# Kernel tuning notes

Hardware: AMD Instinct MI355X
Metric: run time of the kernel (lower is better)

Reference implementation:

```python
import jax, jax.numpy as jnp
import numpy as np
from jax import lax

N, P = 64, 7
C1, H1 = 256, 56
C2, H2 = 512, 28
C3, H3 = 1024, 14
HID1, HID2, HID3 = 256, 768, 1792
MLP1, MLP2, OUT = 3584, 1792, 512


def setup_inputs() -> dict:
    key = jax.random.key(0)
    ks = jax.random.split(key, 32)
    x1 = jax.random.normal(ks[0], (N, C1, H1, H1), jnp.float32)
    x2 = jax.random.normal(ks[1], (N, C2, H2, H2), jnp.float32)
    x3 = jax.random.normal(ks[2], (N, C3, H3, H3), jnp.float32)
    a = jax.random.randint(ks[3], (N, P, 2), 0, 56)
    b = jax.random.randint(ks[4], (N, P, 2), 0, 56)
    lo, hi = jnp.minimum(a, b), jnp.maximum(a, b)
    patchs = jnp.stack([lo[..., 0], hi[..., 0], lo[..., 1], hi[..., 1]], axis=-1)
    drop = jax.random.bernoulli(ks[5], 0.1, (N, P))
    patchs = jnp.where(drop[..., None], 0, patchs).astype(jnp.int32)

    def lin(k, o, i):
        return jax.random.normal(k, (o, i), jnp.float32) * 0.02

    def vec(k, o):
        return jax.random.normal(k, (o,), jnp.float32) * 0.02

    inp = {
        'x1': x1, 'x2': x2, 'x3': x3, 'patchs': patchs,
        # LSTM weights, torch gate order (i,f,g,o); bias = b_ih + b_hh combined
        'l1_wih': lin(ks[6], 4 * HID1, 256),  'l1_whh': lin(ks[7], 4 * HID1, HID1),  'l1_b': vec(ks[8], 4 * HID1),
        'l2_wih': lin(ks[9], 4 * HID2, 768),  'l2_whh': lin(ks[10], 4 * HID2, HID2), 'l2_b': vec(ks[11], 4 * HID2),
        'l3_wih': lin(ks[12], 4 * HID3, 1792),'l3_whh': lin(ks[13], 4 * HID3, HID3), 'l3_b': vec(ks[14], 4 * HID3),
        'aw1': lin(ks[15], MLP1, P * HID3), 'ab1': vec(ks[16], MLP1),
        'aw2': lin(ks[17], MLP2, MLP1),     'ab2': vec(ks[18], MLP2),
        'aw3': lin(ks[19], P, MLP2),        'ab3': vec(ks[20], P),
        'fw':  lin(ks[21], OUT, HID3),      'fb':  vec(ks[22], OUT),
    }
    return inp


def _crop_avg(x, patchs, num, den):
    """Batched data-dependent crop + avg-pool via 2D integral image.
    x: [N,C,H,W]; patchs: [N,P,4] ints (y0,y1,x0,x1) at 56-scale. Returns [N,P,C]."""
    y0 = (patchs[..., 0] * num) // den
    y1 = (patchs[..., 1] * num) // den
    x0 = (patchs[..., 2] * num) // den
    x1 = (patchs[..., 3] * num) // den
    S = jnp.cumsum(jnp.cumsum(x, axis=2), axis=3)
    S = jnp.pad(S, ((0, 0), (0, 0), (1, 0), (1, 0)))  # [N,C,H+1,W+1]
    bidx = jnp.arange(x.shape[0])[:, None]

    def g(Y, X):
        return S[bidx, :, Y, X]  # advanced idx split by ':' -> [N,P,C]

    tot = g(y1 + 1, x1 + 1) - g(y0, x1 + 1) - g(y1 + 1, x0) + g(y0, x0)
    area = ((y1 - y0 + 1) * (x1 - x0 + 1)).astype(x.dtype)[..., None]
    avg = tot / area
    zero = jnp.all(patchs == 0, axis=-1)  # all-zero box -> zero feature
    return jnp.where(zero[..., None], jnp.zeros((), x.dtype), avg)


def _lstm(x, wih, whh, b):
    """Single-layer batch-first LSTM, torch gate order i,f,g,o. x: [N,T,D] -> [N,T,H]."""
    Nb, T, _ = x.shape
    H = whh.shape[1]
    xg = jnp.einsum('ntd,gd->ntg', x, wih) + b  # precompute input gates

    def step(carry, xt):
        h, c = carry
        gates = xt + h @ whh.T
        i, f, g, o = jnp.split(gates, 4, axis=-1)
        c = jax.nn.sigmoid(f) * c + jax.nn.sigmoid(i) * jnp.tanh(g)
        h = jax.nn.sigmoid(o) * jnp.tanh(c)
        return (h, c), h

    h0 = jnp.zeros((Nb, H), x.dtype)
    _, hs = lax.scan(step, (h0, h0), jnp.swapaxes(xg, 0, 1))
    return jnp.swapaxes(hs, 0, 1)


def reference(x1, x2, x3, patchs,
              l1_wih, l1_whh, l1_b, l2_wih, l2_whh, l2_b, l3_wih, l3_whh, l3_b,
              aw1, ab1, aw2, ab2, aw3, ab3, fw, fb):
    local1 = _crop_avg(x1, patchs, 55, 55)                     # [N,7,256]
    rnn1 = _lstm(local1, l1_wih, l1_whh, l1_b)                 # [N,7,256]
    local2 = jnp.concatenate([_crop_avg(x2, patchs, 27, 55), rnn1], axis=2)   # [N,7,768]
    rnn2 = _lstm(local2, l2_wih, l2_whh, l2_b)                 # [N,7,768]
    local3 = jnp.concatenate([_crop_avg(x3, patchs, 13, 55), rnn2], axis=2)   # [N,7,1792]
    rnn3 = _lstm(local3, l3_wih, l3_whh, l3_b)                 # [N,7,1792]
    # attention pooling (dropout = identity in eval)
    flat = rnn3.reshape(rnn3.shape[0], -1)                     # [N,7*1792]
    h = jax.nn.relu(flat @ aw1.T + ab1)
    h = jax.nn.relu(h @ aw2.T + ab2)
    attn = jax.nn.relu(h @ aw3.T + ab3)                        # [N,7]
    alpha = jax.nn.softmax(attn, axis=1)
    feat = jnp.sum(rnn3 * alpha[:, :, None], axis=1)           # [N,1792]
    return feat @ fw.T + fb                                    # [N,512]
```

## Files before the change

kernel.cpp:

```cpp
#include <hip/hip_runtime.h>
#include <hip/hip_bf16.h>
#include <math.h>

#define NB 64
#define PP 7

typedef __attribute__((ext_vector_type(8))) short short8;
typedef __attribute__((ext_vector_type(4))) float f32x4;

static __device__ inline unsigned bf16r(float f) {
    unsigned u = __builtin_bit_cast(unsigned, f);
    u += 0x7fffu + ((u >> 16) & 1u);
    return u >> 16;
}
static __device__ inline unsigned pack2(float a, float b) {
    return bf16r(a) | (bf16r(b) << 16);
}

template<int H, int VEC, int GRP>
__device__ inline void crop_dev(
    int bx, int n, const float* __restrict__ x, const int* __restrict__ patchs,
    float* __restrict__ out, int C, int num, int den, int ldo, int col0)
{
    constexpr int USED = H / VEC;
    constexpr int PPWAVE = 64 / GRP;
    int tid = threadIdx.x, lane = tid & 63, wv = tid >> 6;
    int sub = lane / GRP, xl = lane & (GRP - 1);
    bool act = xl < USED;
    int c = bx * (4 * PPWAVE) + wv * PPWAVE + sub;

    int y0m1[PP], y1s[PP], x0s[PP], x1s[PP], zer[PP];
    float rarea[PP];
    #pragma unroll
    for (int p = 0; p < PP; ++p) {
        int p0 = patchs[(n * PP + p) * 4 + 0];
        int p1 = patchs[(n * PP + p) * 4 + 1];
        int p2 = patchs[(n * PP + p) * 4 + 2];
        int p3 = patchs[(n * PP + p) * 4 + 3];
        int y0 = p0 * num / den, y1 = p1 * num / den;
        int xx0 = p2 * num / den, xx1 = p3 * num / den;
        y0m1[p] = y0 - 1; y1s[p] = y1; x0s[p] = xx0; x1s[p] = xx1;
        rarea[p] = 1.f / (float)((y1 - y0 + 1) * (xx1 - xx0 + 1));
        zer[p] = (p0 | p1 | p2 | p3) == 0;
    }

    const float* pl = x + ((size_t)n * C + c) * (H * H) + (act ? xl * VEC : 0);

    float cc[VEC];
    float lo[PP][VEC], hi[PP][VEC];
    #pragma unroll
    for (int e = 0; e < VEC; ++e) cc[e] = 0.f;
    #pragma unroll
    for (int p = 0; p < PP; ++p)
        #pragma unroll
        for (int e = 0; e < VEC; ++e) { lo[p][e] = 0.f; hi[p][e] = 0.f; }

    #pragma unroll 4
    for (int y = 0; y < H; ++y) {
        float v[VEC];
        if constexpr (VEC == 4) {
            float4 t = *reinterpret_cast<const float4*>(pl + y * H);
            v[0] = t.x; v[1] = t.y; v[2] = t.z; v[3] = t.w;
        } else {
            float2 t = *reinterpret_cast<const float2*>(pl + y * H);
            v[0] = t.x; v[1] = t.y;
        }
        #pragma unroll
        for (int e = 0; e < VEC; ++e) cc[e] += v[e];
        #pragma unroll
        for (int p = 0; p < PP; ++p) {
            #pragma unroll
            for (int e = 0; e < VEC; ++e) {
                lo[p][e] = (y == y0m1[p]) ? cc[e] : lo[p][e];
                hi[p][e] = (y == y1s[p]) ? cc[e] : hi[p][e];
            }
        }
    }

    #pragma unroll
    for (int p = 0; p < PP; ++p) {
        float d = 0.f;
        #pragma unroll
        for (int e = 0; e < VEC; ++e) {
            int col = xl * VEC + e;
            if (col >= x0s[p] && col <= x1s[p]) d += hi[p][e] - lo[p][e];
        }
        #pragma unroll
        for (int off = GRP / 2; off >= 1; off >>= 1)
            d += __shfl_xor(d, off, 64);
        if (act && xl == 0)
            out[(size_t)(n * PP + p) * ldo + col0 + c] = zer[p] ? 0.f : d * rarea[p];
    }
}

__device__ inline void cvt_dev(
    int b, const float* __restrict__ in, uint4* __restrict__ out, int n8)
{
    int idx = b * 256 + threadIdx.x;
    if (idx >= n8) return;
    const float4* p = reinterpret_cast<const float4*>(in) + 2 * (size_t)idx;
    float4 a = p[0], bb = p[1];
    uint4 v;
    v.x = pack2(a.x, a.y); v.y = pack2(a.z, a.w);
    v.z = pack2(bb.x, bb.y); v.w = pack2(bb.z, bb.w);
    out[idx] = v;
}

__global__ __launch_bounds__(256) void prep_kernel(
    const float* __restrict__ x1, const float* __restrict__ x2,
    const float* __restrict__ x3, const int* __restrict__ patchs,
    float* __restrict__ local1, float* __restrict__ local2,
    float* __restrict__ local3,
    const float* __restrict__ l1_whh, uint4* __restrict__ whh1b,
    const float* __restrict__ l2_whh, uint4* __restrict__ whh2b,
    const float* __restrict__ l3_whh, uint4* __restrict__ whh3b)
{
    int b = blockIdx.x;
    if (b < 1024) {
        crop_dev<56, 4, 16>(b & 15, b >> 4, x1, patchs, local1, 256, 55, 55, 256, 0);
    } else if (b < 2048) {
        int bb = b - 1024;
        crop_dev<28, 4, 8>(bb & 15, bb >> 4, x2, patchs, local2, 512, 27, 55, 768, 0);
    } else if (b < 4096) {
        int bb = b - 2048;
        crop_dev<14, 2, 8>(bb & 31, bb >> 5, x3, patchs, local3, 1024, 13, 55, 1792, 0);
    } else if (b < 4224) {
        cvt_dev(b - 4096, l1_whh, whh1b, 32768);
    } else if (b < 5376) {
        cvt_dev(b - 4224, l2_whh, whh2b, 294912);
    } else {
        cvt_dev(b - 5376, l3_whh, whh3b, 1605632);
    }
}

template<int BN, bool WBF>
__global__ __launch_bounds__(256) void gemm_kernel(
    const float* __restrict__ X, int ldx,
    const void* __restrict__ Wp, int K,
    const float* __restrict__ bias,
    float* __restrict__ out, int ldo,
    int kchunk, int partial)
{
    constexpr int NF = BN / 64;
    __shared__ short Xs[64][72];
    __shared__ short Ws[BN][72];
    int tid = threadIdx.x;
    int lane = tid & 63, wv = tid >> 6;
    int m0 = blockIdx.y * 64;
    int o0 = blockIdx.x * BN;
    int z = blockIdx.z;
    int kbeg = z * kchunk, kend = kbeg + kchunk;

    f32x4 acc[4][NF];
    #pragma unroll
    for (int i = 0; i < 4; ++i)
        #pragma unroll
        for (int j = 0; j < NF; ++j)
            acc[i][j] = (f32x4){0.f, 0.f, 0.f, 0.f};

    for (int kb = kbeg; kb < kend; kb += 64) {
        #pragma unroll
        for (int i = 0; i < 2; ++i) {
            int cch = tid + 256 * i;
            int r = cch >> 3, col = (cch & 7) * 8;
            const float* src = X + (size_t)(m0 + r) * ldx + kb + col;
            float4 a = *reinterpret_cast<const float4*>(src);
            float4 b = *reinterpret_cast<const float4*>(src + 4);
            uint4 v;
            v.x = pack2(a.x, a.y); v.y = pack2(a.z, a.w);
            v.z = pack2(b.x, b.y); v.w = pack2(b.z, b.w);
            *reinterpret_cast<uint4*>(&Xs[r][col]) = v;
        }
        #pragma unroll
        for (int i = 0; i < 2 * NF; ++i) {
            int cch = tid + 256 * i;
            int r = cch >> 3, col = (cch & 7) * 8;
            if constexpr (WBF) {
                const short* srcw = (const short*)Wp + (size_t)(o0 + r) * K + kb + col;
                *reinterpret_cast<uint4*>(&Ws[r][col]) =
                    *reinterpret_cast<const uint4*>(srcw);
            } else {
                const float* srcw = (const float*)Wp + (size_t)(o0 + r) * K + kb + col;
                float4 c = *reinterpret_cast<const float4*>(srcw);
                float4 d = *reinterpret_cast<const float4*>(srcw + 4);
                uint4 w;
                w.x = pack2(c.x, c.y); w.y = pack2(c.z, c.w);
                w.z = pack2(d.x, d.y); w.w = pack2(d.z, d.w);
                *reinterpret_cast<uint4*>(&Ws[r][col]) = w;
            }
        }
        __syncthreads();
        #pragma unroll
        for (int kk = 0; kk < 64; kk += 32) {
            int ro = lane & 15, kof = kk + (lane >> 4) * 8;
            short8 b[NF];
            #pragma unroll
            for (int j = 0; j < NF; ++j)
                b[j] = *reinterpret_cast<const short8*>(
                    &Ws[wv * (BN / 4) + 16 * j + ro][kof]);
            #pragma unroll
            for (int i = 0; i < 4; ++i) {
                short8 a = *reinterpret_cast<const short8*>(&Xs[16 * i + ro][kof]);
                #pragma unroll
                for (int j = 0; j < NF; ++j)
                    acc[i][j] = __builtin_amdgcn_mfma_f32_16x16x32_bf16(
                        a, b[j], acc[i][j], 0, 0, 0);
            }
        }
        __syncthreads();
    }

    float* dst = out;
    if (partial) dst += (size_t)z * (gridDim.y * 64) * ldo;
    int mr = (lane >> 4) * 4;
    #pragma unroll
    for (int j = 0; j < NF; ++j) {
        int o = o0 + wv * (BN / 4) + 16 * j + (lane & 15);
        float bv = (!partial && bias) ? bias[o] : 0.f;
        #pragma unroll
        for (int i = 0; i < 4; ++i) {
            #pragma unroll
            for (int r = 0; r < 4; ++r) {
                int m = m0 + 16 * i + mr + r;
                dst[(size_t)m * ldo + o] = acc[i][j][r] + bv;
            }
        }
    }
}

__global__ __launch_bounds__(256) void reduce_kernel(
    const float* __restrict__ partial, int S, int M, int O,
    const float* __restrict__ bias, int relu, float* __restrict__ out)
{
    int idx = blockIdx.x * 256 + threadIdx.x;
    int tot = M * O;
    if (idx >= tot) return;
    float v = bias[idx % O];
    for (int s = 0; s < S; ++s) v += partial[(size_t)s * tot + idx];
    if (relu) v = fmaxf(v, 0.f);
    out[idx] = v;
}

__global__ __launch_bounds__(256) void lstm_cell_kernel(
    const float* __restrict__ partial, int S,
    const float* __restrict__ xgt, int ldxg,
    float* __restrict__ h, float* __restrict__ c,
    float* __restrict__ dest, int Hd, int ldd, int first)
{
    int idx = blockIdx.x * 256 + threadIdx.x;
    int q = Hd >> 2;
    if (idx >= NB * q) return;
    int n = idx / q, j4 = (idx - n * q) * 4;
    int H4 = 4 * Hd;

    f32x4 g[4];
    #pragma unroll
    for (int gi = 0; gi < 4; ++gi)
        g[gi] = *reinterpret_cast<const f32x4*>(xgt + (size_t)n * ldxg + gi * Hd + j4);
    if (!first) {
        for (int s = 0; s < S; ++s) {
            const float* pr = partial + ((size_t)s * NB + n) * H4;
            #pragma unroll
            for (int gi = 0; gi < 4; ++gi)
                g[gi] += *reinterpret_cast<const f32x4*>(pr + gi * Hd + j4);
        }
    }
    f32x4 cp = (f32x4){0.f, 0.f, 0.f, 0.f};
    if (!first) cp = *reinterpret_cast<const f32x4*>(c + (size_t)n * Hd + j4);

    f32x4 cn, hn;
    #pragma unroll
    for (int k = 0; k < 4; ++k) {
        float si = 1.f / (1.f + expf(-g[0][k]));
        float sf = 1.f / (1.f + expf(-g[1][k]));
        float so = 1.f / (1.f + expf(-g[3][k]));
        float cc = sf * cp[k] + si * tanhf(g[2][k]);
        cn[k] = cc;
        hn[k] = so * tanhf(cc);
    }
    *reinterpret_cast<f32x4*>(c + (size_t)n * Hd + j4) = cn;
    *reinterpret_cast<f32x4*>(h + (size_t)n * Hd + j4) = hn;
    *reinterpret_cast<f32x4*>(dest + (size_t)n * ldd + j4) = hn;
}

__global__ __launch_bounds__(256) void attn_fused_kernel(
    const float* __restrict__ h2, const float* __restrict__ aw3,
    const float* __restrict__ ab3, const float* __restrict__ rnn3,
    float* __restrict__ feat)
{
    int n = blockIdx.x;
    int tid = threadIdx.x, lane = tid & 63, wv = tid >> 6;
    __shared__ float logit[PP];
    __shared__ float alpha[PP];
    for (int p = wv; p < PP; p += 4) {
        float s = 0.f;
        for (int k = lane; k < 1792; k += 64)
            s += h2[n * 1792 + k] * aw3[p * 1792 + k];
        #pragma unroll
        for (int off = 32; off; off >>= 1) s += __shfl_down(s, off, 64);
        if (lane == 0) logit[p] = fmaxf(s + ab3[p], 0.f);
    }
    __syncthreads();
    if (tid == 0) {
        float a[PP], mx = -1e30f;
        for (int p = 0; p < PP; ++p) { a[p] = logit[p]; mx = fmaxf(mx, a[p]); }
        float s = 0.f;
        for (int p = 0; p < PP; ++p) { a[p] = expf(a[p] - mx); s += a[p]; }
        for (int p = 0; p < PP; ++p) alpha[p] = a[p] / s;
    }
    __syncthreads();
    for (int j = tid; j < 1792; j += 256) {
        float s = 0.f;
        #pragma unroll
        for (int p = 0; p < PP; ++p)
            s += rnn3[((size_t)n * PP + p) * 1792 + j] * alpha[p];
        feat[(size_t)n * 1792 + j] = s;
    }
}


extern "C" void kernel_launch(void* const* d_in, const int* in_sizes, int n_in,
                              void* d_out, int out_size, void* d_ws, size_t ws_size,
                              hipStream_t stream) {
    const float* x1 = (const float*)d_in[0];
    const float* x2 = (const float*)d_in[1];
    const float* x3 = (const float*)d_in[2];
    const int* patchs = (const int*)d_in[3];
    const float* l1_wih = (const float*)d_in[4];
    const float* l1_whh = (const float*)d_in[5];
    const float* l1_b   = (const float*)d_in[6];
    const float* l2_wih = (const float*)d_in[7];
    const float* l2_whh = (const float*)d_in[8];
    const float* l2_b   = (const float*)d_in[9];
    const float* l3_wih = (const float*)d_in[10];
    const float* l3_whh = (const float*)d_in[11];
    const float* l3_b   = (const float*)d_in[12];
    const float* aw1 = (const float*)d_in[13];
    const float* ab1 = (const float*)d_in[14];
    const float* aw2 = (const float*)d_in[15];
    const float* ab2 = (const float*)d_in[16];
    const float* aw3 = (const float*)d_in[17];
    const float* ab3 = (const float*)d_in[18];
    const float* fw  = (const float*)d_in[19];
    const float* fb  = (const float*)d_in[20];
    float* out = (float*)d_out;

    float* ws = (float*)d_ws;
    float* local1 = ws;
    float* local2 = local1 + 114688;
    float* local3 = local2 + 344064;
    float* rnn3   = local3;
    float* xg     = local3 + 802816;
    float* partial= xg + 3211264;
    float* hbuf   = partial + 3211264;
    float* cbuf   = hbuf + 114688;
    float* h1     = cbuf + 114688;
    float* h2     = h1 + 229376;
    float* feat   = h2 + 114688;
    float* wb     = feat + 114688;
    short* whh1b  = (short*)wb;
    short* whh2b  = (short*)(wb + 131072);
    short* whh3b  = (short*)(wb + 131072 + 1179648);

    prep_kernel<<<11648, 256, 0, stream>>>(
        x1, x2, x3, patchs, local1, local2, local3,
        l1_whh, (uint4*)whh1b, l2_whh, (uint4*)whh2b, l3_whh, (uint4*)whh3b);

    {
        int H = 256, H4 = 1024;
        gemm_kernel<64, false><<<dim3(16, 7, 1), 256, 0, stream>>>(
            local1, 256, l1_wih, 256, l1_b, xg, H4, 256, 0);
        for (int t = 0; t < PP; ++t) {
            if (t > 0)
                gemm_kernel<64, true><<<dim3(16, 1, 4), 256, 0, stream>>>(
                    hbuf, H, whh1b, H, nullptr, partial, H4, 64, 1);
            lstm_cell_kernel<<<(NB * H / 4 + 255) / 256, 256, 0, stream>>>(
                partial, 4, xg + (size_t)t * H4, PP * H4,
                hbuf, cbuf, local2 + (size_t)t * 768 + 512, H, PP * 768, t == 0);
        }
    }
    {
        int H = 768, H4 = 3072;
        gemm_kernel<64, false><<<dim3(48, 7, 1), 256, 0, stream>>>(
            local2, 768, l2_wih, 768, l2_b, xg, H4, 768, 0);
        for (int t = 0; t < PP; ++t) {
            if (t > 0)
                gemm_kernel<64, true><<<dim3(48, 1, 6), 256, 0, stream>>>(
                    hbuf, H, whh2b, H, nullptr, partial, H4, 128, 1);
            lstm_cell_kernel<<<(NB * H / 4 + 255) / 256, 256, 0, stream>>>(
                partial, 6, xg + (size_t)t * H4, PP * H4,
                hbuf, cbuf, local3 + (size_t)t * 1792 + 1024, H, PP * 1792, t == 0);
        }
    }
    {
        int H = 1792, H4 = 7168;
        gemm_kernel<128, false><<<dim3(56, 7, 1), 256, 0, stream>>>(
            local3, 1792, l3_wih, 1792, l3_b, xg, H4, 1792, 0);
        for (int t = 0; t < PP; ++t) {
            if (t > 0)
                gemm_kernel<128, true><<<dim3(56, 1, 7), 256, 0, stream>>>(
                    hbuf, H, whh3b, H, nullptr, partial, H4, 256, 1);
            lstm_cell_kernel<<<(NB * H / 4 + 255) / 256, 256, 0, stream>>>(
                partial, 7, xg + (size_t)t * H4, PP * H4,
                hbuf, cbuf, rnn3 + (size_t)t * 1792, H, PP * 1792, t == 0);
        }
    }

    gemm_kernel<64, false><<<dim3(56, 1, 14), 256, 0, stream>>>(
        rnn3, 12544, aw1, 12544, nullptr, partial, 3584, 896, 1);
    reduce_kernel<<<(64 * 3584 + 255) / 256, 256, 0, stream>>>(
        partial, 14, 64, 3584, ab1, 1, h1);
    gemm_kernel<64, false><<<dim3(28, 1, 7), 256, 0, stream>>>(
        h1, 3584, aw2, 3584, nullptr, partial, 1792, 512, 1);
    reduce_kernel<<<(64 * 1792 + 255) / 256, 256, 0, stream>>>(
        partial, 7, 64, 1792, ab2, 1, h2);
    attn_fused_kernel<<<NB, 256, 0, stream>>>(h2, aw3, ab3, rnn3, feat);
    gemm_kernel<64, false><<<dim3(8, 1, 7), 256, 0, stream>>>(
        feat, 1792, fw, 1792, nullptr, partial, 512, 256, 1);
    reduce_kernel<<<(64 * 512 + 255) / 256, 256, 0, stream>>>(
        partial, 7, 64, 512, fb, 0, out);
}
```

Before: 608.6 us.

## Split crop column-sum scan across row blocks with shuffle prefix combine

```diff
diff --git a/kernel.cpp b/kernel.cpp
--- a/kernel.cpp
+++ b/kernel.cpp
@@ -17,19 +17,25 @@
     return bf16r(a) | (bf16r(b) << 16);
 }
 
-template<int H, int VEC, int GRP>
+template<int H, int VEC, int CL, int RB, int GRP>
 __device__ inline void crop_dev(
     int bx, int n, const float* __restrict__ x, const int* __restrict__ patchs,
     float* __restrict__ out, int C, int num, int den, int ldo, int col0)
 {
-    constexpr int USED = H / VEC;
+    constexpr int R = H / RB;
+    constexpr int ACT = CL * RB;
     constexpr int PPWAVE = 64 / GRP;
     int tid = threadIdx.x, lane = tid & 63, wv = tid >> 6;
-    int sub = lane / GRP, xl = lane & (GRP - 1);
-    bool act = xl < USED;
+    int sub = (lane & (GRP - 1)) == lane ? 0 : 0;
+    int pl = lane & (GRP - 1);
+    sub = lane / GRP;
+    bool act = pl < ACT;
+    int pls = act ? pl : 0;
+    int cl = pls % CL, rb = pls / CL;
     int c = bx * (4 * PPWAVE) + wv * PPWAVE + sub;
 
-    int y0m1[PP], y1s[PP], x0s[PP], x1s[PP], zer[PP];
+    int ylo_loc[PP], yhi_loc[PP], x0s[PP], x1s[PP], zer[PP];
+    int mlo[PP], mhi[PP];
     float rarea[PP];
     #pragma unroll
     for (int p = 0; p < PP; ++p) {
@@ -39,30 +45,35 @@
         int p3 = patchs[(n * PP + p) * 4 + 3];
         int y0 = p0 * num / den, y1 = p1 * num / den;
         int xx0 = p2 * num / den, xx1 = p3 * num / den;
-        y0m1[p] = y0 - 1; y1s[p] = y1; x0s[p] = xx0; x1s[p] = xx1;
+        ylo_loc[p] = (y0 - 1) - rb * R;
+        yhi_loc[p] = y1 - rb * R;
+        mlo[p] = (unsigned)ylo_loc[p] < (unsigned)R;
+        mhi[p] = (unsigned)yhi_loc[p] < (unsigned)R;
+        x0s[p] = xx0; x1s[p] = xx1;
         rarea[p] = 1.f / (float)((y1 - y0 + 1) * (xx1 - xx0 + 1));
         zer[p] = (p0 | p1 | p2 | p3) == 0;
     }
 
-    const float* pl = x + ((size_t)n * C + c) * (H * H) + (act ? xl * VEC : 0);
+    const float* pl_ptr = x + ((size_t)n * C + c) * (H * H)
+                            + (size_t)rb * R * H + cl * VEC;
 
     float cc[VEC];
-    float lo[PP][VEC], hi[PP][VEC];
+    float llo[PP][VEC], lhi[PP][VEC];
     #pragma unroll
     for (int e = 0; e < VEC; ++e) cc[e] = 0.f;
     #pragma unroll
     for (int p = 0; p < PP; ++p)
         #pragma unroll
-        for (int e = 0; e < VEC; ++e) { lo[p][e] = 0.f; hi[p][e] = 0.f; }
-
-    #pragma unroll 4
-    for (int y = 0; y < H; ++y) {
+        for (int e = 0; e < VEC; ++e) { llo[p][e] = 0.f; lhi[p][e] = 0.f; }
+
+    #pragma unroll
+    for (int yl = 0; yl < R; ++yl) {
         float v[VEC];
         if constexpr (VEC == 4) {
-            float4 t = *reinterpret_cast<const float4*>(pl + y * H);
+            float4 t = *reinterpret_cast<const float4*>(pl_ptr + yl * H);
             v[0] = t.x; v[1] = t.y; v[2] = t.z; v[3] = t.w;
         } else {
-            float2 t = *reinterpret_cast<const float2*>(pl + y * H);
+            float2 t = *reinterpret_cast<const float2*>(pl_ptr + yl * H);
             v[0] = t.x; v[1] = t.y;
         }
         #pragma unroll
@@ -71,9 +82,22 @@
         for (int p = 0; p < PP; ++p) {
             #pragma unroll
             for (int e = 0; e < VEC; ++e) {
-                lo[p][e] = (y == y0m1[p]) ? cc[e] : lo[p][e];
-                hi[p][e] = (y == y1s[p]) ? cc[e] : hi[p][e];
+                llo[p][e] = (yl == ylo_loc[p]) ? cc[e] : llo[p][e];
+                lhi[p][e] = (yl == yhi_loc[p]) ? cc[e] : lhi[p][e];
             }
+        }
+    }
+
+    float pre[VEC];
+    #pragma unroll
+    for (int e = 0; e < VEC; ++e) pre[e] = 0.f;
+    #pragma unroll
+    for (int k = 1; k < RB; ++k) {
+        int src = (rb >= k) ? (lane - k * CL) : lane;
+        #pragma unroll
+        for (int e = 0; e < VEC; ++e) {
+            float t = __shfl(cc[e], src, 64);
+            if (rb >= k) pre[e] += t;
         }
     }
 
@@ -82,13 +106,18 @@
         float d = 0.f;
         #pragma unroll
         for (int e = 0; e < VEC; ++e) {
-            int col = xl * VEC + e;
-            if (col >= x0s[p] && col <= x1s[p]) d += hi[p][e] - lo[p][e];
-        }
+            int col = cl * VEC + e;
+            if (col >= x0s[p] && col <= x1s[p]) {
+                float hv = mhi[p] ? (lhi[p][e] + pre[e]) : 0.f;
+                float lv = mlo[p] ? (llo[p][e] + pre[e]) : 0.f;
+                d += hv - lv;
+            }
+        }
+        if (!act) d = 0.f;
         #pragma unroll
         for (int off = GRP / 2; off >= 1; off >>= 1)
             d += __shfl_xor(d, off, 64);
-        if (act && xl == 0)
+        if (act && pl == 0)
             out[(size_t)(n * PP + p) * ldo + col0 + c] = zer[p] ? 0.f : d * rarea[p];
     }
 }
@@ -116,20 +145,23 @@
     const float* __restrict__ l3_whh, uint4* __restrict__ whh3b)
 {
     int b = blockIdx.x;
-    if (b < 1024) {
-        crop_dev<56, 4, 16>(b & 15, b >> 4, x1, patchs, local1, 256, 55, 55, 256, 0);
-    } else if (b < 2048) {
-        int bb = b - 1024;
-        crop_dev<28, 4, 8>(bb & 15, bb >> 4, x2, patchs, local2, 512, 27, 55, 768, 0);
-    } else if (b < 4096) {
-        int bb = b - 2048;
-        crop_dev<14, 2, 8>(bb & 31, bb >> 5, x3, patchs, local3, 1024, 13, 55, 1792, 0);
-    } else if (b < 4224) {
-        cvt_dev(b - 4096, l1_whh, whh1b, 32768);
-    } else if (b < 5376) {
-        cvt_dev(b - 4224, l2_whh, whh2b, 294912);
+    if (b < 4096) {
+        crop_dev<56, 4, 14, 4, 64>(b & 63, b >> 6, x1, patchs, local1,
+                                   256, 55, 55, 256, 0);
+    } else if (b < 8192) {
+        int bb = b - 4096;
+        crop_dev<28, 4, 7, 4, 32>(bb & 63, bb >> 6, x2, patchs, local2,
+                                  512, 27, 55, 768, 0);
+    } else if (b < 12288) {
+        int bb = b - 8192;
+        crop_dev<14, 2, 7, 2, 16>(bb & 63, bb >> 6, x3, patchs, local3,
+                                  1024, 13, 55, 1792, 0);
+    } else if (b < 12416) {
+        cvt_dev(b - 12288, l1_whh, whh1b, 32768);
+    } else if (b < 13568) {
+        cvt_dev(b - 12416, l2_whh, whh2b, 294912);
     } else {
-        cvt_dev(b - 5376, l3_whh, whh3b, 1605632);
+        cvt_dev(b - 13568, l3_whh, whh3b, 1605632);
     }
 }
 
@@ -362,7 +394,7 @@
     short* whh2b  = (short*)(wb + 131072);
     short* whh3b  = (short*)(wb + 131072 + 1179648);
 
-    prep_kernel<<<11648, 256, 0, stream>>>(
+    prep_kernel<<<19840, 256, 0, stream>>>(
         x1, x2, x3, patchs, local1, local2, local3,
         l1_whh, (uint4*)whh1b, l2_whh, (uint4*)whh2b, l3_whh, (uint4*)whh3b);
 
```

After: 617.9 us. About the same (+1.5%).

## Fuse LSTM recurrent GEMM with cell update via last-block atomic counter

Applied to the files above, without the earlier changes.

```diff
diff --git a/kernel.cpp b/kernel.cpp
--- a/kernel.cpp
+++ b/kernel.cpp
@@ -113,7 +113,8 @@
     float* __restrict__ local3,
     const float* __restrict__ l1_whh, uint4* __restrict__ whh1b,
     const float* __restrict__ l2_whh, uint4* __restrict__ whh2b,
-    const float* __restrict__ l3_whh, uint4* __restrict__ whh3b)
+    const float* __restrict__ l3_whh, uint4* __restrict__ whh3b,
+    int* __restrict__ cnt)
 {
     int b = blockIdx.x;
     if (b < 1024) {
@@ -128,8 +129,11 @@
         cvt_dev(b - 4096, l1_whh, whh1b, 32768);
     } else if (b < 5376) {
         cvt_dev(b - 4224, l2_whh, whh2b, 294912);
+    } else if (b < 11648) {
+        cvt_dev(b - 5376, l3_whh, whh3b, 1605632);
     } else {
-        cvt_dev(b - 5376, l3_whh, whh3b, 1605632);
+        int idx = (b - 11648) * 256 + threadIdx.x;
+        if (idx < 1056) cnt[idx] = 0;
     }
 }
 
@@ -228,6 +232,99 @@
     }
 }
 
+__global__ __launch_bounds__(256) void lstm_rec_kernel(
+    const float* __restrict__ hprev, const short* __restrict__ whhb, int H,
+    const float* __restrict__ xgt, int ldxg,
+    float* __restrict__ partial, int S, int kchunk,
+    int* __restrict__ cnt,
+    float* __restrict__ hnew, float* __restrict__ cbuf,
+    float* __restrict__ dest, int ldd)
+{
+    __shared__ short Xs[64][72];
+    __shared__ short Ws[64][72];
+    __shared__ int lastf;
+    int tid = threadIdx.x, lane = tid & 63, wv = tid >> 6;
+    int jt = blockIdx.x, z = blockIdx.z;
+    int j0 = jt * 16;
+    int kbeg = z * kchunk, kend = kbeg + kchunk;
+
+    f32x4 acc[4];
+    #pragma unroll
+    for (int i = 0; i < 4; ++i) acc[i] = (f32x4){0.f, 0.f, 0.f, 0.f};
+
+    for (int kb = kbeg; kb < kend; kb += 64) {
+        #pragma unroll
+        for (int i = 0; i < 2; ++i) {
+            int cch = tid + 256 * i;
+            int r = cch >> 3, col = (cch & 7) * 8;
+            const float* src = hprev + (size_t)r * H + kb + col;
+            float4 a = *reinterpret_cast<const float4*>(src);
+            float4 b = *reinterpret_cast<const float4*>(src + 4);
+            uint4 v;
+            v.x = pack2(a.x, a.y); v.y = pack2(a.z, a.w);
+            v.z = pack2(b.x, b.y); v.w = pack2(b.z, b.w);
+            *reinterpret_cast<uint4*>(&Xs[r][col]) = v;
+            int wr = (r >> 4) * H + j0 + (r & 15);
+            const short* srcw = whhb + (size_t)wr * H + kb + col;
+            *reinterpret_cast<uint4*>(&Ws[r][col]) =
+                *reinterpret_cast<const uint4*>(srcw);
+        }
+        __syncthreads();
+        #pragma unroll
+        for (int kk = 0; kk < 64; kk += 32) {
+            int ro = lane & 15, kof = kk + (lane >> 4) * 8;
+            short8 b = *reinterpret_cast<const short8*>(&Ws[wv * 16 + ro][kof]);
+            #pragma unroll
+            for (int i = 0; i < 4; ++i) {
+                short8 a = *reinterpret_cast<const short8*>(&Xs[16 * i + ro][kof]);
+                acc[i] = __builtin_amdgcn_mfma_f32_16x16x32_bf16(a, b, acc[i], 0, 0, 0);
+            }
+        }
+        __syncthreads();
+    }
+
+    float* pb = partial + (size_t)(jt * S + z) * 4096;
+    int mr = (lane >> 4) * 4;
+    int o = wv * 16 + (lane & 15);
+    #pragma unroll
+    for (int i = 0; i < 4; ++i)
+        #pragma unroll
+        for (int r = 0; r < 4; ++r)
+            pb[(16 * i + mr + r) * 64 + o] = acc[i][r];
+
+    __threadfence();
+    __syncthreads();
+    if (tid == 0) lastf = (atomicAdd(cnt + jt, 1) == S - 1);
+    __syncthreads();
+    if (!lastf) return;
+    __threadfence();
+
+    int n = tid >> 2, u4 = (tid & 3) * 4;
+    f32x4 g[4];
+    #pragma unroll
+    for (int gate = 0; gate < 4; ++gate) {
+        g[gate] = *reinterpret_cast<const f32x4*>(
+            xgt + (size_t)n * ldxg + gate * H + j0 + u4);
+        for (int s = 0; s < S; ++s)
+            g[gate] += *reinterpret_cast<const f32x4*>(
+                partial + (size_t)(jt * S + s) * 4096 + n * 64 + gate * 16 + u4);
+    }
+    f32x4 cp = *reinterpret_cast<const f32x4*>(cbuf + (size_t)n * H + j0 + u4);
+    f32x4 cn, hn;
+    #pragma unroll
+    for (int k = 0; k < 4; ++k) {
+        float si = 1.f / (1.f + expf(-g[0][k]));
+        float sf = 1.f / (1.f + expf(-g[1][k]));
+        float so = 1.f / (1.f + expf(-g[3][k]));
+        float cc = sf * cp[k] + si * tanhf(g[2][k]);
+        cn[k] = cc;
+        hn[k] = so * tanhf(cc);
+    }
+    *reinterpret_cast<f32x4*>(cbuf + (size_t)n * H + j0 + u4) = cn;
+    *reinterpret_cast<f32x4*>(hnew + (size_t)n * H + j0 + u4) = hn;
+    *reinterpret_cast<f32x4*>(dest + (size_t)n * ldd + j0 + u4) = hn;
+}
+
 __global__ __launch_bounds__(256) void reduce_kernel(
     const float* __restrict__ partial, int S, int M, int O,
     const float* __restrict__ bias, int relu, float* __restrict__ out)
@@ -241,40 +338,28 @@
     out[idx] = v;
 }
 
-__global__ __launch_bounds__(256) void lstm_cell_kernel(
-    const float* __restrict__ partial, int S,
+__global__ __launch_bounds__(256) void lstm_cell0_kernel(
     const float* __restrict__ xgt, int ldxg,
     float* __restrict__ h, float* __restrict__ c,
-    float* __restrict__ dest, int Hd, int ldd, int first)
+    float* __restrict__ dest, int Hd, int ldd)
 {
     int idx = blockIdx.x * 256 + threadIdx.x;
     int q = Hd >> 2;
     if (idx >= NB * q) return;
     int n = idx / q, j4 = (idx - n * q) * 4;
-    int H4 = 4 * Hd;
 
     f32x4 g[4];
     #pragma unroll
     for (int gi = 0; gi < 4; ++gi)
         g[gi] = *reinterpret_cast<const f32x4*>(xgt + (size_t)n * ldxg + gi * Hd + j4);
-    if (!first) {
-        for (int s = 0; s < S; ++s) {
-            const float* pr = partial + ((size_t)s * NB + n) * H4;
-            #pragma unroll
-            for (int gi = 0; gi < 4; ++gi)
-                g[gi] += *reinterpret_cast<const f32x4*>(pr + gi * Hd + j4);
-        }
-    }
-    f32x4 cp = (f32x4){0.f, 0.f, 0.f, 0.f};
-    if (!first) cp = *reinterpret_cast<const f32x4*>(c + (size_t)n * Hd + j4);
-
     f32x4 cn, hn;
     #pragma unroll
     for (int k = 0; k < 4; ++k) {
         float si = 1.f / (1.f + expf(-g[0][k]));
         float sf = 1.f / (1.f + expf(-g[1][k]));
         float so = 1.f / (1.f + expf(-g[3][k]));
-        float cc = sf * cp[k] + si * tanhf(g[2][k]);
+        float cc = si * tanhf(g[2][k]);
+        (void)sf;
         cn[k] = cc;
         hn[k] = so * tanhf(cc);
     }
@@ -352,8 +437,9 @@
     float* rnn3   = local3;
     float* xg     = local3 + 802816;
     float* partial= xg + 3211264;
-    float* hbuf   = partial + 3211264;
-    float* cbuf   = hbuf + 114688;
+    float* hbufA  = partial + 3211264;
+    float* hbufB  = hbufA + 114688;
+    float* cbuf   = hbufB + 114688;
     float* h1     = cbuf + 114688;
     float* h2     = h1 + 229376;
     float* feat   = h2 + 114688;
@@ -361,48 +447,58 @@
     short* whh1b  = (short*)wb;
     short* whh2b  = (short*)(wb + 131072);
     short* whh3b  = (short*)(wb + 131072 + 1179648);
-
-    prep_kernel<<<11648, 256, 0, stream>>>(
+    int*   cnt    = (int*)(wb + 131072 + 1179648 + 6422528);
+
+    prep_kernel<<<11653, 256, 0, stream>>>(
         x1, x2, x3, patchs, local1, local2, local3,
-        l1_whh, (uint4*)whh1b, l2_whh, (uint4*)whh2b, l3_whh, (uint4*)whh3b);
-
+        l1_whh, (uint4*)whh1b, l2_whh, (uint4*)whh2b, l3_whh, (uint4*)whh3b,
+        cnt);
+
+    struct L { int H, S, kchunk, jt, cntbase; const float* wih; const float* b;
+               const short* whhb; const float* Xbuf; float* dest; int destHT; int col0; };
     {
         int H = 256, H4 = 1024;
         gemm_kernel<64, false><<<dim3(16, 7, 1), 256, 0, stream>>>(
             local1, 256, l1_wih, 256, l1_b, xg, H4, 256, 0);
-        for (int t = 0; t < PP; ++t) {
-            if (t > 0)
-                gemm_kernel<64, true><<<dim3(16, 1, 4), 256, 0, stream>>>(
-                    hbuf, H, whh1b, H, nullptr, partial, H4, 64, 1);
-            lstm_cell_kernel<<<(NB * H / 4 + 255) / 256, 256, 0, stream>>>(
-                partial, 4, xg + (size_t)t * H4, PP * H4,
-                hbuf, cbuf, local2 + (size_t)t * 768 + 512, H, PP * 768, t == 0);
+        lstm_cell0_kernel<<<16, 256, 0, stream>>>(
+            xg, PP * H4, hbufA, cbuf, local2 + 512, H, PP * 768);
+        for (int t = 1; t < PP; ++t) {
+            const float* hp = (t & 1) ? hbufA : hbufB;
+            float* hw = (t & 1) ? hbufB : hbufA;
+            lstm_rec_kernel<<<dim3(16, 1, 4), 256, 0, stream>>>(
+                hp, whh1b, H, xg + (size_t)t * H4, PP * H4,
+                partial, 4, 64, cnt + (t - 1) * 16,
+                hw, cbuf, local2 + (size_t)t * 768 + 512, PP * 768);
         }
     }
     {
         int H = 768, H4 = 3072;
         gemm_kernel<64, false><<<dim3(48, 7, 1), 256, 0, stream>>>(
             local2, 768, l2_wih, 768, l2_b, xg, H4, 768, 0);
-        for (int t = 0; t < PP; ++t) {
-            if (t > 0)
-                gemm_kernel<64, true><<<dim3(48, 1, 6), 256, 0, stream>>>(
-                    hbuf, H, whh2b, H, nullptr, partial, H4, 128, 1);
-            lstm_cell_kernel<<<(NB * H / 4 + 255) / 256, 256, 0, stream>>>(
-                partial, 6, xg + (size_t)t * H4, PP * H4,
-                hbuf, cbuf, local3 + (size_t)t * 1792 + 1024, H, PP * 1792, t == 0);
+        lstm_cell0_kernel<<<48, 256, 0, stream>>>(
+            xg, PP * H4, hbufA, cbuf, local3 + 1024, H, PP * 1792);
+        for (int t = 1; t < PP; ++t) {
+            const float* hp = (t & 1) ? hbufA : hbufB;
+            float* hw = (t & 1) ? hbufB : hbufA;
+            lstm_rec_kernel<<<dim3(48, 1, 6), 256, 0, stream>>>(
+                hp, whh2b, H, xg + (size_t)t * H4, PP * H4,
+                partial, 6, 128, cnt + 96 + (t - 1) * 48,
+                hw, cbuf, local3 + (size_t)t * 1792 + 1024, PP * 1792);
         }
     }
     {
         int H = 1792, H4 = 7168;
         gemm_kernel<128, false><<<dim3(56, 7, 1), 256, 0, stream>>>(
             local3, 1792, l3_wih, 1792, l3_b, xg, H4, 1792, 0);
-        for (int t = 0; t < PP; ++t) {
-            if (t > 0)
-                gemm_kernel<128, true><<<dim3(56, 1, 7), 256, 0, stream>>>(
-                    hbuf, H, whh3b, H, nullptr, partial, H4, 256, 1);
-            lstm_cell_kernel<<<(NB * H / 4 + 255) / 256, 256, 0, stream>>>(
-                partial, 7, xg + (size_t)t * H4, PP * H4,
-                hbuf, cbuf, rnn3 + (size_t)t * 1792, H, PP * 1792, t == 0);
+        lstm_cell0_kernel<<<112, 256, 0, stream>>>(
+            xg, PP * H4, hbufA, cbuf, rnn3, H, PP * 1792);
+        for (int t = 1; t < PP; ++t) {
+            const float* hp = (t & 1) ? hbufA : hbufB;
+            float* hw = (t & 1) ? hbufB : hbufA;
+            lstm_rec_kernel<<<dim3(112, 1, 7), 256, 0, stream>>>(
+                hp, whh3b, H, xg + (size_t)t * H4, PP * H4,
+                partial, 7, 256, cnt + 384 + (t - 1) * 112,
+                hw, cbuf, rnn3 + (size_t)t * 1792, PP * 1792);
         }
     }
 
```

After: 1.385 ms. +127.7%, slower.
